# Kernel optimization log

Measured on AMD Instinct MI355X. Metric: run time of the kernel, lower is better.

## Reference

```python
import jax, jax.numpy as jnp
import numpy as np

OUT_FEATURES = 11008
IN_FEATURES = 4096
GROUP_SIZE = 32
NUM_GROUPS = OUT_FEATURES * IN_FEATURES // GROUP_SIZE        # 1,409,024
NUM_PACKED = NUM_GROUPS * (GROUP_SIZE // 8 * 3)              # 16,908,288 bytes


def block_dequantize_3bit(weight_q3, weight_norm):
    """Unpack 3-bit codes (8 values per 3 bytes) and dequantize to fp32."""
    p = weight_q3.reshape(-1, 3).astype(jnp.int32)  # [N/8, 3] bytes
    b0, b1, b2 = p[:, 0], p[:, 1], p[:, 2]
    q = jnp.stack([
        b0 & 7,
        (b0 >> 3) & 7,
        ((b0 >> 6) & 3) | ((b1 & 1) << 2),
        (b1 >> 1) & 7,
        (b1 >> 4) & 7,
        ((b1 >> 7) & 1) | ((b2 & 3) << 1),
        (b2 >> 2) & 7,
        (b2 >> 5) & 7,
    ], axis=-1)                                     # [N/8, 8] codes in 0..7
    q = q.reshape(NUM_GROUPS, GROUP_SIZE).astype(jnp.float32)
    norm = weight_norm.astype(jnp.float32)[:, None]  # [num_groups, 1]
    w = (q / 7.0) * 2.0 * norm - norm                # map [0,7] -> [-norm, norm]
    return w.reshape(OUT_FEATURES, IN_FEATURES)


def setup_inputs() -> dict:
    key = jax.random.key(0)
    k1, k2, k3, k4 = jax.random.split(key, 4)
    x = jax.random.normal(k1, (4, 128, IN_FEATURES), dtype=jnp.float32)
    weight_q3 = jax.random.randint(k2, (NUM_PACKED,), 0, 256, dtype=jnp.int32)
    weight_norm = (jax.random.uniform(k3, (NUM_GROUPS,), dtype=jnp.float32) * 0.1 + 0.01).astype(jnp.float16)
    bias = jax.random.normal(k4, (OUT_FEATURES,), dtype=jnp.float32) * 0.02
    return {"x": x, "weight_q3": weight_q3, "weight_norm": weight_norm, "bias": bias}


def reference(x, weight_q3, weight_norm, bias):
    w = block_dequantize_3bit(weight_q3, weight_norm)  # [out, in] fp32
    return jnp.einsum('bsd,od->bso', x, w) + bias
```

## Files before the change

kernel.cpp:

```cpp
#include <hip/hip_runtime.h>
#include <hip/hip_fp16.h>

#define M_TOTAL 512
#define N_TOTAL 11008
#define K_TOTAL 4096
#define BM 128
#define BN 64
#define BK 64
#define NT (K_TOTAL / BK)
#define LDK 72

typedef short bf16x8 __attribute__((ext_vector_type(8)));
typedef float f32x4 __attribute__((ext_vector_type(4)));

__device__ __forceinline__ unsigned int pack2_bf16(float f0, float f1) {
    unsigned int u0 = __builtin_bit_cast(unsigned int, f0) + 0x8000u;
    unsigned int u1 = __builtin_bit_cast(unsigned int, f1) + 0x8000u;
    return (u0 >> 16) | (u1 & 0xFFFF0000u);
}

__device__ __forceinline__ void async_ld16(void* lds, const void* g) {
    __builtin_amdgcn_global_load_lds(
        (const __attribute__((address_space(1))) unsigned int*)g,
        (__attribute__((address_space(3))) unsigned int*)lds, 16, 0, 0);
}

__device__ __forceinline__ int detect_mode_wave(const void* __restrict__ wn) {
    const int lane = threadIdx.x & 63;
    const unsigned short* u16 = (const unsigned short*)wn;
    const float* f32p = (const float*)wn;
    const float vb = __builtin_bit_cast(float, (unsigned int)u16[lane] << 16);
    const float vh = __half2float(__builtin_bit_cast(__half, u16[lane]));
    const float vf = f32p[lane];
    const unsigned long long mb = __ballot(vb > 0.005f && vb < 0.12f);
    const unsigned long long mh = __ballot(vh > 0.005f && vh < 0.12f);
    (void)vf;
    return (mb == ~0ull) ? 2 : ((mh == ~0ull) ? 1 : 0);
}

__global__ void __launch_bounds__(256)
convert_x_kernel(const float* __restrict__ x, unsigned short* __restrict__ xb) {
    const int i = (blockIdx.x * 256 + threadIdx.x) * 4;
    const float4 v = *(const float4*)&x[i];
    *(uint2*)&xb[i] = make_uint2(pack2_bf16(v.x, v.y), pack2_bf16(v.z, v.w));
}

__global__ void __launch_bounds__(256, 3)
l3b_gemm_pipe(const unsigned short* __restrict__ xb, const int* __restrict__ wq,
              const void* __restrict__ wnorm, const float* __restrict__ bias,
              float* __restrict__ out)
{
    __shared__ unsigned short As[2][BM * 64];
    __shared__ unsigned short Bs[2][BN * 64];

    const int tid  = threadIdx.x;
    const int mode = detect_mode_wave(wnorm);

    const int bid = blockIdx.x;
    const int w   = (bid & 7) * 86 + (bid >> 3);
    const int m0  = (w & 3) * BM;
    const int n0  = (w >> 2) * BN;

    const int wid  = tid >> 6;
    const int lane = tid & 63;
    const int quad = lane >> 4;
    const int lm   = lane & 15;
    const int wm   = (wid >> 1) * 64;
    const int wn_  = (wid & 1) * 32;

    const int arow0 = wid * 8 + (lane >> 3);
    const int acol  = ((lane & 7) ^ ((lane >> 3) & 7)) * 8;
    const int aslot = (lane & 7) * 8;

    const int gl   = tid >> 1;
    const int hf   = tid & 1;
    const int bn_l = gl >> 1;
    const int kg   = gl & 1;
    const int sw   = bn_l & 7;
    const int c0   = kg * 4 + hf * 2;
    const int ldsB0 = (bn_l << 6) + (((c0    ) ^ sw) << 3);
    const int ldsB1 = (bn_l << 6) + (((c0 + 1) ^ sw) << 3);

    auto stageA = [&](int it, int buf) {
#pragma unroll
        for (int j = 0; j < 4; ++j) {
            const int row = arow0 + j * 32;
            async_ld16(&As[buf][(row << 6) + aslot],
                       &xb[(size_t)(m0 + row) * K_TOTAL + it * 64 + acol]);
        }
    };

    auto loadNorm = [&](int g) -> float {
        if (mode == 0)      return ((const float*)wnorm)[g];
        else if (mode == 1) return __half2float(((const __half*)wnorm)[g]);
        else                return __builtin_bit_cast(float,
                               (unsigned int)((const unsigned short*)wnorm)[g] << 16);
    };
    auto loadB = [&](int it, int2& w0, int2& w1, int2& w2, float& nrm) {
        const int g    = (n0 + bn_l) * (K_TOTAL / 32) + it * 2 + kg;
        const int base = g * 12 + hf * 6;
        w0 = *(const int2*)&wq[base];
        w1 = *(const int2*)&wq[base + 2];
        w2 = *(const int2*)&wq[base + 4];
        nrm = loadNorm(g);
    };
    auto decodeB = [&](int2 w0, int2 w1, int2 w2, float nrm, int buf) {
        const float a = nrm * (2.0f / 7.0f);
        const float b = -nrm;
        const unsigned int bits0 =
            (unsigned)w0.x | ((unsigned)w0.y << 8) | ((unsigned)w1.x << 16);
        const unsigned int bits1 =
            (unsigned)w1.y | ((unsigned)w2.x << 8) | ((unsigned)w2.y << 16);
        unsigned int packs[8];
#pragma unroll
        for (int t3 = 0; t3 < 2; ++t3) {
            const unsigned int bits = t3 ? bits1 : bits0;
#pragma unroll
            for (int j = 0; j < 4; ++j) {
                const float f0 = fmaf((float)((bits >> (6 * j)) & 7), a, b);
                const float f1 = fmaf((float)((bits >> (6 * j + 3)) & 7), a, b);
                packs[t3 * 4 + j] = pack2_bf16(f0, f1);
            }
        }
        *(uint4*)&Bs[buf][ldsB0] = make_uint4(packs[0], packs[1], packs[2], packs[3]);
        *(uint4*)&Bs[buf][ldsB1] = make_uint4(packs[4], packs[5], packs[6], packs[7]);
    };

    f32x4 acc[4][2];
#pragma unroll
    for (int i = 0; i < 4; ++i)
#pragma unroll
        for (int j = 0; j < 2; ++j) acc[i][j] = (f32x4){0.f, 0.f, 0.f, 0.f};

    auto mfmaTile = [&](const unsigned short* Asb, const unsigned short* Bsb) {
#pragma unroll
        for (int ks = 0; ks < 2; ++ks) {
            const int cswz = (((ks * 4 + quad) ^ (lm & 7)) << 3);
            bf16x8 aF[4], bF[2];
#pragma unroll
            for (int mi = 0; mi < 4; ++mi)
                aF[mi] = *(const bf16x8*)&Asb[((wm + mi * 16 + lm) << 6) + cswz];
#pragma unroll
            for (int ni = 0; ni < 2; ++ni)
                bF[ni] = *(const bf16x8*)&Bsb[((wn_ + ni * 16 + lm) << 6) + cswz];
#pragma unroll
            for (int mi = 0; mi < 4; ++mi)
#pragma unroll
                for (int ni = 0; ni < 2; ++ni)
                    acc[mi][ni] = __builtin_amdgcn_mfma_f32_16x16x32_bf16(
                        aF[mi], bF[ni], acc[mi][ni], 0, 0, 0);
        }
    };

    int2 w0a, w1a, w2a; float na;
    int2 w0b, w1b, w2b; float nb;

    stageA(0, 0);
    loadB(0, w0a, w1a, w2a, na);
    decodeB(w0a, w1a, w2a, na, 0);
    loadB(1, w0b, w1b, w2b, nb);
    __syncthreads();

    for (int it = 0; it < NT; it += 2) {
        if (it + 1 < NT) stageA(it + 1, 1);
        if (it + 2 < NT) loadB(it + 2, w0a, w1a, w2a, na);
        if (it + 1 < NT) decodeB(w0b, w1b, w2b, nb, 1);
        mfmaTile(As[0], Bs[0]);
        __syncthreads();

        if (it + 2 < NT) stageA(it + 2, 0);
        if (it + 3 < NT) loadB(it + 3, w0b, w1b, w2b, nb);
        if (it + 2 < NT) decodeB(w0a, w1a, w2a, na, 0);
        mfmaTile(As[1], Bs[1]);
        __syncthreads();
    }

#pragma unroll
    for (int ni = 0; ni < 2; ++ni) {
        const int o  = n0 + wn_ + ni * 16 + lm;
        const float bv = bias[o];
#pragma unroll
        for (int mi = 0; mi < 4; ++mi) {
#pragma unroll
            for (int r = 0; r < 4; ++r) {
                const int m = m0 + wm + mi * 16 + quad * 4 + r;
                out[m * N_TOTAL + o] = acc[mi][ni][r] + bv;
            }
        }
    }
}

__global__ void __launch_bounds__(256)
l3b_gemm_kernel(const float* __restrict__ x, const int* __restrict__ wq,
                const void* __restrict__ wnorm, const float* __restrict__ bias,
                float* __restrict__ out)
{
    __shared__ unsigned short As[128 * LDK];
    __shared__ unsigned short Bs[64 * LDK];

    const int mode = detect_mode_wave(wnorm);
    const int tid  = threadIdx.x;
    const int m0   = blockIdx.y * 128;
    const int n0   = blockIdx.x * 64;
    const int wid  = tid >> 6;
    const int lane = tid & 63;
    const int quad = lane >> 4;
    const int lm   = lane & 15;
    const int wm   = (wid >> 1) * 64;
    const int wn   = (wid & 1) * 32;

    f32x4 acc[4][2];
#pragma unroll
    for (int i = 0; i < 4; ++i)
#pragma unroll
        for (int j = 0; j < 2; ++j) acc[i][j] = (f32x4){0.f, 0.f, 0.f, 0.f};

    const int ar = tid >> 4;
    const int ac = (tid & 15) * 4;
    const int gin      = tid >> 1;
    const int half     = tid & 1;
    const int bn_local = gin >> 1;
    const int bkg      = gin & 1;

    for (int it = 0; it < NT; ++it) {
        const int k0 = it * BK;
        __syncthreads();
#pragma unroll
        for (int p = 0; p < 8; ++p) {
            const int row = p * 16 + ar;
            const float4 v = *(const float4*)&x[(m0 + row) * K_TOTAL + k0 + ac];
            *(uint2*)&As[row * LDK + ac] =
                make_uint2(pack2_bf16(v.x, v.y), pack2_bf16(v.z, v.w));
        }
        {
            const int g    = (n0 + bn_local) * (K_TOTAL / 32) + it * 2 + bkg;
            const int base = g * 12 + half * 6;
            const int2 w0 = *(const int2*)&wq[base];
            const int2 w1 = *(const int2*)&wq[base + 2];
            const int2 w2 = *(const int2*)&wq[base + 4];
            float nrm;
            if (mode == 0)      nrm = ((const float*)wnorm)[g];
            else if (mode == 1) nrm = __half2float(((const __half*)wnorm)[g]);
            else                nrm = __builtin_bit_cast(float,
                                    (unsigned int)((const unsigned short*)wnorm)[g] << 16);
            const float a = nrm * (2.0f / 7.0f);
            const float b = -nrm;
            const unsigned int bits0 =
                (unsigned)w0.x | ((unsigned)w0.y << 8) | ((unsigned)w1.x << 16);
            const unsigned int bits1 =
                (unsigned)w1.y | ((unsigned)w2.x << 8) | ((unsigned)w2.y << 16);
            unsigned int packs[8];
#pragma unroll
            for (int t3 = 0; t3 < 2; ++t3) {
                const unsigned int bits = t3 ? bits1 : bits0;
#pragma unroll
                for (int j = 0; j < 4; ++j) {
                    const float f0 = fmaf((float)((bits >> (6 * j)) & 7), a, b);
                    const float f1 = fmaf((float)((bits >> (6 * j + 3)) & 7), a, b);
                    packs[t3 * 4 + j] = pack2_bf16(f0, f1);
                }
            }
            unsigned int* dst = (unsigned int*)&Bs[bn_local * LDK + bkg * 32 + half * 16];
            *(uint4*)dst       = make_uint4(packs[0], packs[1], packs[2], packs[3]);
            *(uint4*)(dst + 4) = make_uint4(packs[4], packs[5], packs[6], packs[7]);
        }
        __syncthreads();
#pragma unroll
        for (int ks = 0; ks < 2; ++ks) {
            const int kb = ks * 32 + quad * 8;
            bf16x8 aF[4], bF[2];
#pragma unroll
            for (int mi = 0; mi < 4; ++mi)
                aF[mi] = *(const bf16x8*)&As[(wm + mi * 16 + lm) * LDK + kb];
#pragma unroll
            for (int ni = 0; ni < 2; ++ni)
                bF[ni] = *(const bf16x8*)&Bs[(wn + ni * 16 + lm) * LDK + kb];
#pragma unroll
            for (int mi = 0; mi < 4; ++mi)
#pragma unroll
                for (int ni = 0; ni < 2; ++ni)
                    acc[mi][ni] = __builtin_amdgcn_mfma_f32_16x16x32_bf16(
                        aF[mi], bF[ni], acc[mi][ni], 0, 0, 0);
        }
    }
#pragma unroll
    for (int ni = 0; ni < 2; ++ni) {
        const int o  = n0 + wn + ni * 16 + lm;
        const float bv = bias[o];
#pragma unroll
        for (int mi = 0; mi < 4; ++mi)
#pragma unroll
            for (int r = 0; r < 4; ++r) {
                const int m = m0 + wm + mi * 16 + quad * 4 + r;
                out[m * N_TOTAL + o] = acc[mi][ni][r] + bv;
            }
    }
}

extern "C" void kernel_launch(void* const* d_in, const int* in_sizes, int n_in,
                              void* d_out, int out_size, void* d_ws, size_t ws_size,
                              hipStream_t stream) {
    const float* x    = (const float*)d_in[0];
    const int*   wq   = (const int*)d_in[1];
    const void*  wn   = d_in[2];
    const float* bias = (const float*)d_in[3];
    float* out = (float*)d_out;

    const size_t need = 256 + (size_t)M_TOTAL * K_TOTAL * 2;
    if (ws_size >= need) {
        unsigned short* xb = (unsigned short*)((char*)d_ws + 256);
        convert_x_kernel<<<(M_TOTAL * K_TOTAL / 4) / 256, 256, 0, stream>>>(x, xb);
        l3b_gemm_pipe<<<(M_TOTAL / BM) * (N_TOTAL / BN), 256, 0, stream>>>(
            xb, wq, wn, bias, out);
    } else {
        dim3 grid(N_TOTAL / 64, M_TOTAL / 128);
        l3b_gemm_kernel<<<grid, 256, 0, stream>>>(x, wq, wn, bias, out);
    }
}
```

Before: 198.6 us.

## Switch GEMM to fp16 MFMA with bit-trick 3-bit decode and partial waitcnt barriers

Converts activations to fp16 instead of bf16 and decodes 3-bit weights by ORing the code into an fp16 mantissa, then applying one packed half2 FMA, replacing per-element int-to-float conversions and fp32 FMAs. MFMA switches to the f16 variant and is wrapped in s_setprio. __syncthreads is replaced with explicit vmcnt(3)/lgkmcnt(0) waits plus s_barrier so in-flight B global loads need not drain at each barrier. This risks fp16 range/precision issues and a synchronization bug if the vmcnt count doesn't match the outstanding loads.

```diff
diff --git a/kernel.cpp b/kernel.cpp
--- a/kernel.cpp
+++ b/kernel.cpp
@@ -11,6 +11,7 @@
 #define LDK 72
 
 typedef short bf16x8 __attribute__((ext_vector_type(8)));
+typedef _Float16 fp16x8 __attribute__((ext_vector_type(8)));
 typedef float f32x4 __attribute__((ext_vector_type(4)));
 
 __device__ __forceinline__ unsigned int pack2_bf16(float f0, float f1) {
@@ -42,7 +43,10 @@
 convert_x_kernel(const float* __restrict__ x, unsigned short* __restrict__ xb) {
     const int i = (blockIdx.x * 256 + threadIdx.x) * 4;
     const float4 v = *(const float4*)&x[i];
-    *(uint2*)&xb[i] = make_uint2(pack2_bf16(v.x, v.y), pack2_bf16(v.z, v.w));
+    const __half2 p0 = __floats2half2_rn(v.x, v.y);
+    const __half2 p1 = __floats2half2_rn(v.z, v.w);
+    *(uint2*)&xb[i] = make_uint2(__builtin_bit_cast(unsigned int, p0),
+                                 __builtin_bit_cast(unsigned int, p1));
 }
 
 __global__ void __launch_bounds__(256, 3)
@@ -105,8 +109,10 @@
         nrm = loadNorm(g);
     };
     auto decodeB = [&](int2 w0, int2 w1, int2 w2, float nrm, int buf) {
-        const float a = nrm * (2.0f / 7.0f);
-        const float b = -nrm;
+        const float af = nrm * (16.0f / 7.0f);
+        const float bf = nrm * (-23.0f / 7.0f);
+        const __half2 A2 = __float2half2_rn(af);
+        const __half2 B2 = __float2half2_rn(bf);
         const unsigned int bits0 =
             (unsigned)w0.x | ((unsigned)w0.y << 8) | ((unsigned)w1.x << 16);
         const unsigned int bits1 =
@@ -117,9 +123,11 @@
             const unsigned int bits = t3 ? bits1 : bits0;
 #pragma unroll
             for (int j = 0; j < 4; ++j) {
-                const float f0 = fmaf((float)((bits >> (6 * j)) & 7), a, b);
-                const float f1 = fmaf((float)((bits >> (6 * j + 3)) & 7), a, b);
-                packs[t3 * 4 + j] = pack2_bf16(f0, f1);
+                const unsigned int q0 = (bits >> (6 * j)) & 7u;
+                const unsigned int q1 = (bits >> (6 * j + 3)) & 7u;
+                const unsigned int y  = 0x3C003C00u | (q0 << 7) | (q1 << 23);
+                const __half2 wv = __hfma2(__builtin_bit_cast(__half2, y), A2, B2);
+                packs[t3 * 4 + j] = __builtin_bit_cast(unsigned int, wv);
             }
         }
         *(uint4*)&Bs[buf][ldsB0] = make_uint4(packs[0], packs[1], packs[2], packs[3]);
@@ -136,19 +144,21 @@
 #pragma unroll
         for (int ks = 0; ks < 2; ++ks) {
             const int cswz = (((ks * 4 + quad) ^ (lm & 7)) << 3);
-            bf16x8 aF[4], bF[2];
+            fp16x8 aF[4], bF[2];
 #pragma unroll
             for (int mi = 0; mi < 4; ++mi)
-                aF[mi] = *(const bf16x8*)&Asb[((wm + mi * 16 + lm) << 6) + cswz];
+                aF[mi] = *(const fp16x8*)&Asb[((wm + mi * 16 + lm) << 6) + cswz];
 #pragma unroll
             for (int ni = 0; ni < 2; ++ni)
-                bF[ni] = *(const bf16x8*)&Bsb[((wn_ + ni * 16 + lm) << 6) + cswz];
+                bF[ni] = *(const fp16x8*)&Bsb[((wn_ + ni * 16 + lm) << 6) + cswz];
+            __builtin_amdgcn_s_setprio(1);
 #pragma unroll
             for (int mi = 0; mi < 4; ++mi)
 #pragma unroll
                 for (int ni = 0; ni < 2; ++ni)
-                    acc[mi][ni] = __builtin_amdgcn_mfma_f32_16x16x32_bf16(
+                    acc[mi][ni] = __builtin_amdgcn_mfma_f32_16x16x32_f16(
                         aF[mi], bF[ni], acc[mi][ni], 0, 0, 0);
+            __builtin_amdgcn_s_setprio(0);
         }
     };
 
@@ -163,16 +173,28 @@
 
     for (int it = 0; it < NT; it += 2) {
         if (it + 1 < NT) stageA(it + 1, 1);
+        __builtin_amdgcn_sched_barrier(0);
         if (it + 2 < NT) loadB(it + 2, w0a, w1a, w2a, na);
         if (it + 1 < NT) decodeB(w0b, w1b, w2b, nb, 1);
         mfmaTile(As[0], Bs[0]);
-        __syncthreads();
+        if (it + 2 < NT) {
+            asm volatile("s_waitcnt vmcnt(3) lgkmcnt(0)" ::: "memory");
+        } else {
+            asm volatile("s_waitcnt vmcnt(0) lgkmcnt(0)" ::: "memory");
+        }
+        __builtin_amdgcn_s_barrier();
 
         if (it + 2 < NT) stageA(it + 2, 0);
+        __builtin_amdgcn_sched_barrier(0);
         if (it + 3 < NT) loadB(it + 3, w0b, w1b, w2b, nb);
         if (it + 2 < NT) decodeB(w0a, w1a, w2a, na, 0);
         mfmaTile(As[1], Bs[1]);
-        __syncthreads();
+        if (it + 3 < NT) {
+            asm volatile("s_waitcnt vmcnt(3) lgkmcnt(0)" ::: "memory");
+        } else {
+            asm volatile("s_waitcnt vmcnt(0) lgkmcnt(0)" ::: "memory");
+        }
+        __builtin_amdgcn_s_barrier();
     }
 
 #pragma unroll
```

After: 199.2 us. Within noise of the previous version (+0.3%).
